# Optimization experiments

Hardware: AMD Instinct MI355X
Metric: run time of the kernel (lower is better)

Reference implementation:

```python
import jax, jax.numpy as jnp
import numpy as np


def _lstm_layer(x, W_ih, W_hh, b_ih, b_hh):
    # x: [B, T, D_in]; W_ih: [4H, D_in]; W_hh: [4H, H]; gate order i,f,g,o (PyTorch).
    B, T, _ = x.shape
    H = W_hh.shape[1]
    # Precompute all input projections once (batched GEMM over time).
    x_proj = jnp.einsum('bti,gi->btg', x, W_ih) + b_ih + b_hh  # [B, T, 4H]
    x_proj = jnp.transpose(x_proj, (1, 0, 2))                  # [T, B, 4H]

    def step(carry, xt):
        h, c = carry
        gates = xt + h @ W_hh.T                                # [B, 4H]
        i, f, g, o = jnp.split(gates, 4, axis=-1)
        i = jax.nn.sigmoid(i)
        f = jax.nn.sigmoid(f)
        g = jnp.tanh(g)
        o = jax.nn.sigmoid(o)
        c = f * c + i * g
        h = o * jnp.tanh(c)
        return (h, c), h

    h0 = jnp.zeros((B, H), dtype=x.dtype)
    c0 = jnp.zeros((B, H), dtype=x.dtype)
    (_, _), hs = jax.lax.scan(step, (h0, c0), x_proj)          # hs: [T, B, H]
    return jnp.transpose(hs, (1, 0, 2))                        # [B, T, H]


def setup_inputs() -> dict:
    key = jax.random.key(0)
    ks = jax.random.split(key, 12)
    B, T, D, H, O = 4096, 512, 5, 50, 1
    s = 1.0 / np.sqrt(H)  # torch default init scale
    u = lambda k, shape: jax.random.uniform(k, shape, jnp.float32, -s, s)
    return {
        'x': jax.random.normal(ks[0], (B, T, D), jnp.float32),
        'W_ih0': u(ks[1], (4 * H, D)),
        'W_hh0': u(ks[2], (4 * H, H)),
        'b_ih0': u(ks[3], (4 * H,)),
        'b_hh0': u(ks[4], (4 * H,)),
        'W_ih1': u(ks[5], (4 * H, H)),
        'W_hh1': u(ks[6], (4 * H, H)),
        'b_ih1': u(ks[7], (4 * H,)),
        'b_hh1': u(ks[8], (4 * H,)),
        'W_lin': u(ks[9], (O, H)),
        'b_lin': u(ks[10], (O,)),
    }


def reference(x, W_ih0, W_hh0, b_ih0, b_hh0, W_ih1, W_hh1, b_ih1, b_hh1, W_lin, b_lin):
    # 2-layer LSTM (eval mode: inter-layer dropout inactive) + linear head on last step.
    h1 = _lstm_layer(x, W_ih0, W_hh0, b_ih0, b_hh0)   # [B, T, H]
    h2 = _lstm_layer(h1, W_ih1, W_hh1, b_ih1, b_hh1)  # [B, T, H]
    last = h2[:, -1, :]                               # [B, H]
    return last @ W_lin.T + b_lin                     # [B, 1]
```

## Files before the change

kernel.cpp:

```cpp
#include <hip/hip_runtime.h>


#define NB 16
#define BLK 512
#define TT 512
#define LOG2E 1.44269504088896340736f
#define SA 72
#define SXR 264

typedef _Float16 half8 __attribute__((ext_vector_type(8)));
typedef __attribute__((ext_vector_type(4))) float f32x4;

#define MFMAH(a, b, c) __builtin_amdgcn_mfma_f32_16x16x32_f16((a), (b), (c), 0, 0, 0)

__device__ __forceinline__ float fexp2(float x) { return __builtin_amdgcn_exp2f(x); }
__device__ __forceinline__ float frcp(float x)  { return __builtin_amdgcn_rcpf(x); }

#define CELL_UPDATE(ACCX, DST, GUARD)                                       \
    _Pragma("unroll")                                                       \
    for (int r = 0; r < 4; ++r) {                                           \
        float eu = fexp2(ACCX[0][r]);                                \
        float ew = fexp2(ACCX[1][r]);                                \
        float ev = fexp2(ACCX[2][r]);                     \
        float ey = fexp2(ACCX[3][r]);                                \
        float pu = 1.f + eu, pw = 1.f + ew, pv = 1.f + ev;                  \
        float P  = pu * pv;                                                 \
        float rD = frcp(P * pw);                                            \
        float N  = cst[r] * P + (2.f - pv) * pw;                            \
        float cn = N * rD;                                                  \
        cst[r] = cn;                                                        \
        float za = fminf(cn * (-2.f * LOG2E), 80.f);                        \
        float ez = fexp2(za);                                               \
        float pz = 1.f + ez, py = 1.f + ey;                                 \
        float rQ = frcp(py * pz);                                           \
        float h  = (2.f - pz) * rQ;                                         \
        if (GUARD) (DST)[(4 * c + r) * SA + j] = (_Float16)h;               \
    }

#define TICK(T, RB1, WB1)                                                   \
    {                                                                       \
        if (grp == 0) {                                                     \
            if ((T) < TT) {                                                 \
                __builtin_amdgcn_s_setprio(1);                              \
                half8 a0 = *(const half8*)&sA0[r3][ln * SA + 0 + 8 * c];    \
                half8 a1 = *(const half8*)&sA0[r3][ln * SA + 32 + 8 * c];   \
                             \
                if ((T) < TT - 1 && xlane) {                                \
                    int tl1 = ((T) + 1) & 31;                               \
                    sA0[w3][xb * SA + 50 + xd] =                            \
                        (_Float16)sX[xb * SXR + tl1 * 8 + xd];              \
                }                                                           \
                f32x4 acc[4];                                               \
                _Pragma("unroll")                                           \
                for (int p = 0; p < 4; ++p) {                               \
                    acc[p] = MFMAH(a0, bfr[p][0], bias4[p]);                \
                    acc[p] = MFMAH(a1, bfr[p][1], acc[p]);                  \
                }                                                           \
                __builtin_amdgcn_s_setprio(0);                              \
                CELL_UPDATE(acc, &sA0[w3][0], jv)                           \
            }                                                               \
        } else {                                                            \
            if ((T) >= 2) {                                                 \
                __builtin_amdgcn_s_setprio(1);                              \
                half8 a2 = *(const half8*)&sA1[RB1][ln * SA + 0 + 8 * c];   \
                half8 a3 = *(const half8*)&sA1[RB1][ln * SA + 32 + 8 * c];  \
                f32x4 acc[4];                                               \
                _Pragma("unroll")                                           \
                for (int p = 0; p < 4; ++p)                                 \
                    acc[p] = MFMAH(l1a0, bfr[p][0], bias4[p]);              \
                _Pragma("unroll")                                           \
                for (int p = 0; p < 4; ++p)                                 \
                    acc[p] = MFMAH(l1a1, bfr[p][1], acc[p]);                \
                \
                \
                l1a0 = *(const half8*)&sA0[r3][ln * SA + 0 + 8 * c];        \
                l1a1 = *(const half8*)&sA0[r3][ln * SA + 32 + 8 * c];       \
                _Pragma("unroll")                                           \
                for (int p = 0; p < 4; ++p) {                               \
                    acc[p] = MFMAH(a2, bfr[p][2], acc[p]);                  \
                    acc[p] = MFMAH(a3, bfr[p][3], acc[p]);                  \
                }                                                           \
                __builtin_amdgcn_s_setprio(0);                              \
                CELL_UPDATE(acc, &sA1[WB1][0], true)                        \
            } else if ((T) == 1) {                                          \
                l1a0 = *(const half8*)&sA0[r3][ln * SA + 0 + 8 * c];        \
                l1a1 = *(const half8*)&sA0[r3][ln * SA + 32 + 8 * c];       \
            }                                                               \
        }                                                                   \
        __syncthreads();                                                    \
        r3 = w3; w3 = (w3 == 2) ? 0 : (w3 + 1);                             \
    }

#define STAGE(T)                                                            \
    if ((T) < TT - 1) {                                                     \
        _Pragma("unroll")                                                   \
        for (int q = 0; q < 5; ++q) {                                       \
            int e = tid + q * BLK, b_ = e / 160, r_ = e - b_ * 160;         \
            int ts = r_ / 5, d_ = r_ - ts * 5;                              \
            sX[b_ * SXR + ts * 8 + d_] = xr[q];                             \
        }                                                                   \
        if ((T) + 33 < TT) {                                                \
            _Pragma("unroll")                                               \
            for (int q = 0; q < 5; ++q) {                                   \
                int e = tid + q * BLK, b_ = e / 160, r_ = e - b_ * 160;     \
                xr[q] = x[(size_t)(bb0 + b_) * 2560 +                       \
                          (size_t)((T) + 33) * 5 + r_];                     \
            }                                                               \
        }                                                                   \
        __syncthreads();                                                    \
    }

__global__ __launch_bounds__(512, 2) void lstm2_v8(
    const float* __restrict__ x,
    const float* __restrict__ Wih0,
    const float* __restrict__ Whh0,
    const float* __restrict__ bih0,
    const float* __restrict__ bhh0,
    const float* __restrict__ Wih1,
    const float* __restrict__ Whh1,
    const float* __restrict__ bih1,
    const float* __restrict__ bhh1,
    const float* __restrict__ Wlin,
    const float* __restrict__ blin,
    float* __restrict__ out)
{
    __shared__ __align__(16) _Float16 sA0[3][16 * SA];
    __shared__ __align__(16) _Float16 sA1[2][16 * SA];
    __shared__ __align__(16) float sX[16 * SXR];

    const int tid = threadIdx.x;
    const int w = tid >> 6, l = tid & 63, c = l >> 4, ln = l & 15;
    const int grp = w >> 2, wl = w & 3;
    const int bb0 = blockIdx.x * NB;
    const int j = 16 * wl + ln;
    const bool jv = (j < 50);

    const bool xlane = (grp == 0) && (l < 20);
    const int xb = 4 * w + l / 5, xd = l % 5;

    for (int i = tid; i < 3 * 16 * SA; i += BLK) (&sA0[0][0])[i] = (_Float16)0.f;
    for (int i = tid; i < 2 * 16 * SA; i += BLK) (&sA1[0][0])[i] = (_Float16)0.f;

    half8 bfr[4][4];
    f32x4 bias4[4];
#pragma unroll
    for (int p = 0; p < 4; ++p) {
        const float gs = (p == 2) ? (-2.f * LOG2E) : (-LOG2E);
        const int g = p * 50 + j;
#pragma unroll
        for (int s = 0; s < 4; ++s) {
            half8 tb;
#pragma unroll
            for (int jj = 0; jj < 8; ++jj) {
                int k = 32 * s + 8 * c + jj;
                float v = 0.f;
                if (jv) {
                    if (grp == 0) {
                        if (k < 50)      v = Whh0[g * 50 + k];
                        else if (k < 55) v = Wih0[g * 5 + (k - 50)];
                    } else {
                        if (k < 50)                  v = Wih1[g * 50 + k];
                        else if (k >= 64 && k < 114) v = Whh1[g * 50 + (k - 64)];
                    }
                }
                tb[jj] = (_Float16)(v * gs);
            }
            bfr[p][s] = tb;
        }
        float bv = jv ? ((grp == 0) ? (bih0[g] + bhh0[g]) : (bih1[g] + bhh1[g])) : 0.f;
        bv *= gs;
        f32x4 b4; b4[0] = bv; b4[1] = bv; b4[2] = bv; b4[3] = bv;
        bias4[p] = b4;
    }

    float cst[4] = {0.f, 0.f, 0.f, 0.f};
    half8 l1a0 = {}, l1a1 = {};
    int r3 = 2, w3 = 0;

    float xr[5];
#pragma unroll
    for (int q = 0; q < 5; ++q) {
        int e = tid + q * BLK, b = e / 160, r = e - b * 160;
        xr[q] = x[(size_t)(bb0 + b) * 2560 + r];
    }
#pragma unroll
    for (int q = 0; q < 5; ++q) {
        int e = tid + q * BLK, b = e / 160, r = e - b * 160;
        int ts = r / 5, d = r - ts * 5;
        sX[b * SXR + ts * 8 + d] = xr[q];
    }
#pragma unroll
    for (int q = 0; q < 5; ++q) {
        int e = tid + q * BLK, b = e / 160, r = e - b * 160;
        xr[q] = x[(size_t)(bb0 + b) * 2560 + 160 + r];
    }
    __syncthreads();

    if (tid < 80) {
        int b = tid / 5, d = tid - 5 * b;
        sA0[2][b * SA + 50 + d] = (_Float16)x[(size_t)(bb0 + b) * 2560 + d];
    }
    __syncthreads();

    for (int t = 0; t < TT + 2; t += 2) {
        TICK(t, 1, 0)
        if ((t & 31) == 30) { STAGE(t + 1) }
        TICK(t + 1, 0, 1)
    }

    if (tid < NB) {
        float s = blin[0];
#pragma unroll
        for (int jj = 0; jj < 50; ++jj)
            s += Wlin[jj] * (float)sA1[1][tid * SA + jj];
        out[bb0 + tid] = s;
    }
}

extern "C" void kernel_launch(void* const* d_in, const int* in_sizes, int n_in,
                              void* d_out, int out_size, void* d_ws, size_t ws_size,
                              hipStream_t stream) {
    (void)in_sizes; (void)n_in; (void)d_ws; (void)ws_size; (void)out_size;
    const float* x    = (const float*)d_in[0];
    const float* Wih0 = (const float*)d_in[1];
    const float* Whh0 = (const float*)d_in[2];
    const float* bih0 = (const float*)d_in[3];
    const float* bhh0 = (const float*)d_in[4];
    const float* Wih1 = (const float*)d_in[5];
    const float* Whh1 = (const float*)d_in[6];
    const float* bih1 = (const float*)d_in[7];
    const float* bhh1 = (const float*)d_in[8];
    const float* Wlin = (const float*)d_in[9];
    const float* blin = (const float*)d_in[10];

    lstm2_v8<<<dim3(256), dim3(512), 0, stream>>>(
        x, Wih0, Whh0, bih0, bhh0, Wih1, Whh1, bih1, bhh1, Wlin, blin,
        (float*)d_out);
}
```

Before: 352.0 us.

## Use 4-slot layer-0 ring with static indices, FMA-fused gate math, earlier stage sync

Grows the layer-0 hidden-state ring buffer from 3 to 4 slots and unrolls the time loop by 4, so each tick uses compile-time slot indices instead of runtime rotating r3/w3 counters. The gate nonlinearity arithmetic is rewritten with explicit FMAs, which removes a few multiplies and adds per cell. The barrier in the x-staging step now comes before the next global prefetch rather than after it, so the loads can overlap the following ticks. The cost is a little more shared memory and a larger unrolled loop body, which adds register and instruction-cache pressure.

```diff
diff --git a/kernel.cpp b/kernel.cpp
--- a/kernel.cpp
+++ b/kernel.cpp
@@ -23,31 +23,36 @@
         float ew = fexp2(ACCX[1][r]);                                \
         float ev = fexp2(ACCX[2][r]);                     \
         float ey = fexp2(ACCX[3][r]);                                \
-        float pu = 1.f + eu, pw = 1.f + ew, pv = 1.f + ev;                  \
-        float P  = pu * pv;                                                 \
-        float rD = frcp(P * pw);                                            \
-        float N  = cst[r] * P + (2.f - pv) * pw;                            \
+        float pu = 1.f + eu;                                                \
+        float P  = __builtin_fmaf(pu, ev, pu);                              \
+        float PD = __builtin_fmaf(P, ew, P);                                \
+        float s_ = 1.f - ev;                                                \
+        float t2 = __builtin_fmaf(s_, ew, s_);                              \
+        float N  = __builtin_fmaf(cst[r], P, t2);                           \
+        float rD = frcp(PD);                                                \
         float cn = N * rD;                                                  \
         cst[r] = cn;                                                        \
         float za = fminf(cn * (-2.f * LOG2E), 80.f);                        \
         float ez = fexp2(za);                                               \
-        float pz = 1.f + ez, py = 1.f + ey;                                 \
-        float rQ = frcp(py * pz);                                           \
-        float h  = (2.f - pz) * rQ;                                         \
+        float py = 1.f + ey;                                                \
+        float Q  = __builtin_fmaf(py, ez, py);                              \
+        float rQ = frcp(Q);                                                 \
+        float g2 = 1.f - ez;                                                \
+        float h  = g2 * rQ;                                                 \
         if (GUARD) (DST)[(4 * c + r) * SA + j] = (_Float16)h;               \
     }
 
-#define TICK(T, RB1, WB1)                                                   \
+#define TICK(T, RB1, WB1, R4, W4)                                           \
     {                                                                       \
         if (grp == 0) {                                                     \
             if ((T) < TT) {                                                 \
                 __builtin_amdgcn_s_setprio(1);                              \
-                half8 a0 = *(const half8*)&sA0[r3][ln * SA + 0 + 8 * c];    \
-                half8 a1 = *(const half8*)&sA0[r3][ln * SA + 32 + 8 * c];   \
+                half8 a0 = *(const half8*)&sA0[R4][ln * SA + 0 + 8 * c];    \
+                half8 a1 = *(const half8*)&sA0[R4][ln * SA + 32 + 8 * c];   \
                              \
                 if ((T) < TT - 1 && xlane) {                                \
                     int tl1 = ((T) + 1) & 31;                               \
-                    sA0[w3][xb * SA + 50 + xd] =                            \
+                    sA0[W4][xb * SA + 50 + xd] =                            \
                         (_Float16)sX[xb * SXR + tl1 * 8 + xd];              \
                 }                                                           \
                 f32x4 acc[4];                                               \
@@ -57,7 +62,7 @@
                     acc[p] = MFMAH(a1, bfr[p][1], acc[p]);                  \
                 }                                                           \
                 __builtin_amdgcn_s_setprio(0);                              \
-                CELL_UPDATE(acc, &sA0[w3][0], jv)                           \
+                CELL_UPDATE(acc, &sA0[W4][0], jv)                           \
             }                                                               \
         } else {                                                            \
             if ((T) >= 2) {                                                 \
@@ -73,8 +78,8 @@
                     acc[p] = MFMAH(l1a1, bfr[p][1], acc[p]);                \
                 \
                 \
-                l1a0 = *(const half8*)&sA0[r3][ln * SA + 0 + 8 * c];        \
-                l1a1 = *(const half8*)&sA0[r3][ln * SA + 32 + 8 * c];       \
+                l1a0 = *(const half8*)&sA0[R4][ln * SA + 0 + 8 * c];        \
+                l1a1 = *(const half8*)&sA0[R4][ln * SA + 32 + 8 * c];       \
                 _Pragma("unroll")                                           \
                 for (int p = 0; p < 4; ++p) {                               \
                     acc[p] = MFMAH(a2, bfr[p][2], acc[p]);                  \
@@ -83,12 +88,11 @@
                 __builtin_amdgcn_s_setprio(0);                              \
                 CELL_UPDATE(acc, &sA1[WB1][0], true)                        \
             } else if ((T) == 1) {                                          \
-                l1a0 = *(const half8*)&sA0[r3][ln * SA + 0 + 8 * c];        \
-                l1a1 = *(const half8*)&sA0[r3][ln * SA + 32 + 8 * c];       \
+                l1a0 = *(const half8*)&sA0[R4][ln * SA + 0 + 8 * c];        \
+                l1a1 = *(const half8*)&sA0[R4][ln * SA + 32 + 8 * c];       \
             }                                                               \
         }                                                                   \
         __syncthreads();                                                    \
-        r3 = w3; w3 = (w3 == 2) ? 0 : (w3 + 1);                             \
     }
 
 #define STAGE(T)                                                            \
@@ -99,6 +103,7 @@
             int ts = r_ / 5, d_ = r_ - ts * 5;                              \
             sX[b_ * SXR + ts * 8 + d_] = xr[q];                             \
         }                                                                   \
+        __syncthreads();                                                    \
         if ((T) + 33 < TT) {                                                \
             _Pragma("unroll")                                               \
             for (int q = 0; q < 5; ++q) {                                   \
@@ -107,10 +112,9 @@
                           (size_t)((T) + 33) * 5 + r_];                     \
             }                                                               \
         }                                                                   \
-        __syncthreads();                                                    \
-    }
-
-__global__ __launch_bounds__(512, 2) void lstm2_v8(
+    }
+
+__global__ __launch_bounds__(512, 2) void lstm2_v9(
     const float* __restrict__ x,
     const float* __restrict__ Wih0,
     const float* __restrict__ Whh0,
@@ -124,7 +128,7 @@
     const float* __restrict__ blin,
     float* __restrict__ out)
 {
-    __shared__ __align__(16) _Float16 sA0[3][16 * SA];
+    __shared__ __align__(16) _Float16 sA0[4][16 * SA];
     __shared__ __align__(16) _Float16 sA1[2][16 * SA];
     __shared__ __align__(16) float sX[16 * SXR];
 
@@ -138,7 +142,7 @@
     const bool xlane = (grp == 0) && (l < 20);
     const int xb = 4 * w + l / 5, xd = l % 5;
 
-    for (int i = tid; i < 3 * 16 * SA; i += BLK) (&sA0[0][0])[i] = (_Float16)0.f;
+    for (int i = tid; i < 4 * 16 * SA; i += BLK) (&sA0[0][0])[i] = (_Float16)0.f;
     for (int i = tid; i < 2 * 16 * SA; i += BLK) (&sA1[0][0])[i] = (_Float16)0.f;
 
     half8 bfr[4][4];
@@ -175,7 +179,6 @@
 
     float cst[4] = {0.f, 0.f, 0.f, 0.f};
     half8 l1a0 = {}, l1a1 = {};
-    int r3 = 2, w3 = 0;
 
     float xr[5];
 #pragma unroll
@@ -198,15 +201,19 @@
 
     if (tid < 80) {
         int b = tid / 5, d = tid - 5 * b;
-        sA0[2][b * SA + 50 + d] = (_Float16)x[(size_t)(bb0 + b) * 2560 + d];
+        sA0[3][b * SA + 50 + d] = (_Float16)x[(size_t)(bb0 + b) * 2560 + d];
     }
     __syncthreads();
 
-    for (int t = 0; t < TT + 2; t += 2) {
-        TICK(t, 1, 0)
-        if ((t & 31) == 30) { STAGE(t + 1) }
-        TICK(t + 1, 0, 1)
-    }
+    for (int t = 0; t < TT; t += 4) {
+        TICK(t + 0, 1, 0, 3, 0)
+        TICK(t + 1, 0, 1, 0, 1)
+        TICK(t + 2, 1, 0, 1, 2)
+        if ((t & 31) == 28) { STAGE(t + 3) }
+        TICK(t + 3, 0, 1, 2, 3)
+    }
+    TICK(TT,     1, 0, 3, 0)
+    TICK(TT + 1, 0, 1, 0, 1)
 
     if (tid < NB) {
         float s = blin[0];
@@ -233,7 +240,7 @@
     const float* Wlin = (const float*)d_in[9];
     const float* blin = (const float*)d_in[10];
 
-    lstm2_v8<<<dim3(256), dim3(512), 0, stream>>>(
+    lstm2_v9<<<dim3(256), dim3(512), 0, stream>>>(
         x, Wih0, Whh0, bih0, bhh0, Wih1, Whh1, bih1, bhh1, Wlin, blin,
         (float*)d_out);
 }
```

After: 338.3 us. 3.9% less time.
